# Kernel optimization log

Hardware: AMD Instinct MI355X
Metric: run time of the kernel (lower is better)

The kernel has to match this reference:

```python
import jax, jax.numpy as jnp
import numpy as np

H = 8  # num_heads
EPS = 1e-5


def layer_norm(x, g, b):
    mu = jnp.mean(x, axis=-1, keepdims=True)
    var = jnp.mean((x - mu) ** 2, axis=-1, keepdims=True)
    return (x - mu) * jax.lax.rsqrt(var + EPS) * g + b


def setup_inputs() -> dict:
    key = jax.random.key(0)
    ks = jax.random.split(key, 8)
    B, N, C = 2, 2048, 512
    Dff = 2048
    s = 0.02
    x = jax.random.normal(ks[0], (B, N, C), dtype=jnp.float32)
    mask = (jax.random.uniform(ks[1], (N, N)) > 0.5).astype(jnp.float32)
    return {
        "x": x,
        "mask": mask,
        "w_qkv": jax.random.normal(ks[2], (3 * C, C), dtype=jnp.float32) * s,
        "w_proj": jax.random.normal(ks[3], (C, C), dtype=jnp.float32) * s,
        "b_proj": jnp.zeros((C,), jnp.float32),
        "g1": jnp.ones((C,), jnp.float32),
        "beta1": jnp.zeros((C,), jnp.float32),
        "g2": jnp.ones((C,), jnp.float32),
        "beta2": jnp.zeros((C,), jnp.float32),
        "w1": jax.random.normal(ks[4], (Dff, C), dtype=jnp.float32) * s,
        "bm1": jnp.zeros((Dff,), jnp.float32),
        "w2": jax.random.normal(ks[5], (C, Dff), dtype=jnp.float32) * s,
        "bm2": jnp.zeros((C,), jnp.float32),
    }


def attn_block(h, mask, w_qkv, w_proj, b_proj):
    B, N, C = h.shape
    hd = C // H
    scale = hd ** -0.5
    qkv = (h @ w_qkv.T).reshape(B, N, 3, H, hd)
    q, k, v = jnp.moveaxis(qkv, 2, 0)          # each [B, N, H, hd]
    q = q.transpose(0, 2, 1, 3)                 # [B, H, N, hd]
    k = k.transpose(0, 2, 1, 3)
    v = v.transpose(0, 2, 1, 3)
    attn = jnp.einsum("bhnd,bhmd->bhnm", q, k) * scale
    attn = attn * mask                          # multiplicative sparse mask
    attn = jax.nn.softmax(attn, axis=-1)
    o = jnp.einsum("bhnm,bhmd->bhnd", attn, v)
    o = o.transpose(0, 2, 1, 3).reshape(B, N, C)
    return o @ w_proj.T + b_proj


def reference(x, mask, w_qkv, w_proj, b_proj, g1, beta1, g2, beta2, w1, bm1, w2, bm2):
    # pre-norm transformer block, dropout/drop_path disabled (eval)
    y = x + attn_block(layer_norm(x, g1, beta1), mask, w_qkv, w_proj, b_proj)
    h = layer_norm(y, g2, beta2)
    h = jax.nn.gelu(h @ w1.T + bm1, approximate=False)  # torch F.gelu default (erf)
    z = y + (h @ w2.T + bm2)
    return z
```

## Files before the change

kernel.cpp:

```cpp
#include <hip/hip_runtime.h>
#include <cmath>
#include <stdint.h>

#define N_SEQ 2048
#define C_DIM 512
#define BATCH 2
#define NHEAD 8
#define DFF   2048
#define M_ROWS (BATCH * N_SEQ)

typedef unsigned short ushort_t;
typedef unsigned long long u64;
typedef __bf16 bf16x8 __attribute__((ext_vector_type(8)));
typedef float  f32x4  __attribute__((ext_vector_type(4)));
typedef float  f32x16 __attribute__((ext_vector_type(16)));

__device__ __forceinline__ float bf2f(ushort_t u) {
    union { unsigned int i; float f; } v; v.i = ((unsigned int)u) << 16; return v.f;
}
__device__ __forceinline__ ushort_t f2bf_(float f) {
    union { float f; unsigned int i; } v; v.f = f;
    unsigned int r = v.i + 0x7fffu + ((v.i >> 16) & 1u);
    return (ushort_t)(r >> 16);
}
__device__ __forceinline__ unsigned short bfbits(float f) {
    return __builtin_bit_cast(unsigned short, (__bf16)f);
}
__device__ __forceinline__ int get_is32(const unsigned int* g1w) {
    return g1w[0] == 0x3F800000u;
}

__device__ __forceinline__ void load_lds16(const ushort_t* g, ushort_t* lds_wave_base) {
    __builtin_amdgcn_global_load_lds(
        (const __attribute__((address_space(1))) void*)g,
        (__attribute__((address_space(3))) void*)lds_wave_base, 16, 0, 0);
}

__device__ __forceinline__ float gelu_f(float u) {
    float c = u + 0.044715f * u * u * u;
    float E = exp2f(-2.302068545f * c);
    return u / (1.0f + E);
}

template <typename TX, typename TG>
__device__ __forceinline__ void ln_row(int row, int lane, const TX* __restrict__ x,
                                       const TG* __restrict__ g, const TG* __restrict__ b,
                                       ushort_t* __restrict__ out) {
    const TX* xr = x + (size_t)row * C_DIM + lane * 8;
    float v[8];
    if (sizeof(TX) == 2) {
        bf16x8 t = *(const bf16x8*)xr;
        #pragma unroll
        for (int j = 0; j < 8; ++j) v[j] = (float)t[j];
    } else {
        const float4* q = (const float4*)xr;
        float4 a = q[0], c = q[1];
        v[0]=a.x; v[1]=a.y; v[2]=a.z; v[3]=a.w; v[4]=c.x; v[5]=c.y; v[6]=c.z; v[7]=c.w;
    }
    float s = 0.f, sq = 0.f;
    #pragma unroll
    for (int j = 0; j < 8; ++j) { s += v[j]; sq += v[j] * v[j]; }
    #pragma unroll
    for (int m = 1; m < 64; m <<= 1) { s += __shfl_xor(s, m, 64); sq += __shfl_xor(sq, m, 64); }
    float mean = s * (1.0f / C_DIM);
    float var  = fmaxf(sq * (1.0f / C_DIM) - mean * mean, 0.0f);
    float rs = rsqrtf(var + 1e-5f);
    float gv[8], bv[8];
    const TG* gp = g + lane * 8; const TG* bp = b + lane * 8;
    if (sizeof(TG) == 2) {
        bf16x8 tg = *(const bf16x8*)gp, tb = *(const bf16x8*)bp;
        #pragma unroll
        for (int j = 0; j < 8; ++j) { gv[j] = (float)tg[j]; bv[j] = (float)tb[j]; }
    } else {
        const float4* qg = (const float4*)gp; const float4* qb = (const float4*)bp;
        float4 a=qg[0], c=qg[1], d=qb[0], e=qb[1];
        gv[0]=a.x;gv[1]=a.y;gv[2]=a.z;gv[3]=a.w;gv[4]=c.x;gv[5]=c.y;gv[6]=c.z;gv[7]=c.w;
        bv[0]=d.x;bv[1]=d.y;bv[2]=d.z;bv[3]=d.w;bv[4]=e.x;bv[5]=e.y;bv[6]=e.z;bv[7]=e.w;
    }
    bf16x8 o;
    #pragma unroll
    for (int j = 0; j < 8; ++j) o[j] = (__bf16)((v[j] - mean) * rs * gv[j] + bv[j]);
    *(bf16x8*)(out + (size_t)row * C_DIM + lane * 8) = o;
}

__global__ __launch_bounds__(256) void prep_kernel(const unsigned int* __restrict__ g1w,
        const void* w_qkv, const void* w_proj, const void* w1, const void* w2,
        const void* mask, const void* x, const void* g1, const void* b1,
        ushort_t* wq_bf, ushort_t* wp_bf, ushort_t* w1_bf, ushort_t* w2_bf,
        u64* __restrict__ maskM, ushort_t* __restrict__ hout) {
    int is32 = get_is32(g1w);
    int bid = blockIdx.x;
    int wave = threadIdx.x >> 6, lane = threadIdx.x & 63;
    if (bid < 1536) {
        long e = ((long)bid * 256 + threadIdx.x) * 8;
        const void* src; ushort_t* dst; long off;
        if      (e < 786432)  { src = w_qkv; dst = wq_bf;  off = e; }
        else if (e < 1048576) { src = w_proj; dst = wp_bf; off = e - 786432; }
        else if (e < 2097152) { src = w1;    dst = w1_bf;  off = e - 1048576; }
        else                  { src = w2;    dst = w2_bf;  off = e - 2097152; }
        bf16x8 r;
        if (is32) {
            const float4* q = (const float4*)((const float*)src + off);
            float4 a = q[0], b = q[1];
            r[0]=(__bf16)a.x; r[1]=(__bf16)a.y; r[2]=(__bf16)a.z; r[3]=(__bf16)a.w;
            r[4]=(__bf16)b.x; r[5]=(__bf16)b.y; r[6]=(__bf16)b.z; r[7]=(__bf16)b.w;
        } else {
            r = *(const bf16x8*)((const ushort_t*)src + off);
        }
        *(bf16x8*)(dst + off) = r;
    } else if (bid < 2560) {
        int pb = bid - 1536;
        #pragma unroll
        for (int it = 0; it < 16; ++it) {
            int p = pb * 64 + wave * 16 + it;
            int q = p >> 5, kb = p & 31;
            size_t idx = (size_t)q * N_SEQ + kb * 64 + lane;
            bool m = is32 ? (((const float*)mask)[idx] != 0.0f)
                          : ((((const ushort_t*)mask)[idx] & 0x7fffu) != 0);
            u64 bits = __ballot(m);
            if (lane == 0) maskM[(size_t)q * 32 + kb] = bits;
        }
    } else {
        int row = (bid - 2560) * 4 + wave;
        if (is32) ln_row<float, float>(row, lane, (const float*)x, (const float*)g1, (const float*)b1, hout);
        else      ln_row<ushort_t, ushort_t>(row, lane, (const ushort_t*)x, (const ushort_t*)g1, (const ushort_t*)b1, hout);
    }
}

__global__ __launch_bounds__(256) void ln2_kernel(const unsigned int* __restrict__ g1w,
        const ushort_t* __restrict__ y, const void* g, const void* b, ushort_t* out) {
    int row = blockIdx.x * 4 + (threadIdx.x >> 6), lane = threadIdx.x & 63;
    if (get_is32(g1w)) ln_row<ushort_t, float>(row, lane, y, (const float*)g, (const float*)b, out);
    else               ln_row<ushort_t, ushort_t>(row, lane, y, (const ushort_t*)g, (const ushort_t*)b, out);
}

template <int K, int KSPLIT, int BN, bool HAS_BIAS, int ACT, int OUT_MODE>
__global__ __launch_bounds__(256) void gemm_big(const unsigned int* __restrict__ g1w,
        const ushort_t* __restrict__ A, const ushort_t* __restrict__ W,
        const void* __restrict__ bias, void* __restrict__ Cout, int Nout) {
    constexpr int MT = (BN == 128) ? 4 : 2;
    constexpr int KL = K / KSPLIT;
    __shared__ __align__(16) ushort_t As[2][128][32];
    __shared__ __align__(16) ushort_t Bs[2][BN][32];
    int t = threadIdx.x;
    int wave = t >> 6, lane = t & 63, quad = lane >> 4, l16 = lane & 15;
    int wave_m = (BN == 128) ? (wave >> 1) : wave;
    int wave_n = (BN == 128) ? (wave & 1) : 0;
    int row0 = blockIdx.y * 128, col0 = blockIdx.x * BN;
    int kz = (KSPLIT > 1) ? blockIdx.z : 0;
    int kbase = kz * KL;

    f32x4 acc[MT][4] = {};
    int arow = t >> 2, kofs = (t & 3) * 8;

    {
        int kk = kbase + kofs;
        load_lds16(A + (size_t)(row0 + arow) * K + kk,      &As[0][0][0] + wave * 512);
        load_lds16(A + (size_t)(row0 + 64 + arow) * K + kk, &As[0][64][0] + wave * 512);
        load_lds16(W + (size_t)(col0 + arow) * K + kk,      &Bs[0][0][0] + wave * 512);
        if (BN == 128)
            load_lds16(W + (size_t)(col0 + 64 + arow) * K + kk, &Bs[0][64][0] + wave * 512);
    }
    for (int k0 = 0; k0 < KL; k0 += 32) {
        int cur = (k0 >> 5) & 1;
        __syncthreads();
        if (k0 + 32 < KL) {
            int kk = kbase + k0 + 32 + kofs;
            load_lds16(A + (size_t)(row0 + arow) * K + kk,      &As[cur ^ 1][0][0] + wave * 512);
            load_lds16(A + (size_t)(row0 + 64 + arow) * K + kk, &As[cur ^ 1][64][0] + wave * 512);
            load_lds16(W + (size_t)(col0 + arow) * K + kk,      &Bs[cur ^ 1][0][0] + wave * 512);
            if (BN == 128)
                load_lds16(W + (size_t)(col0 + 64 + arow) * K + kk, &Bs[cur ^ 1][64][0] + wave * 512);
        }
        bf16x8 af[MT], bfr[4];
        #pragma unroll
        for (int i = 0; i < MT; ++i)
            af[i] = *(const bf16x8*)&As[cur][wave_m * (MT * 16) + i * 16 + l16][quad * 8];
        #pragma unroll
        for (int j = 0; j < 4; ++j)
            bfr[j] = *(const bf16x8*)&Bs[cur][wave_n * 64 + j * 16 + l16][quad * 8];
        #pragma unroll
        for (int i = 0; i < MT; ++i)
            #pragma unroll
            for (int j = 0; j < 4; ++j)
                acc[i][j] = __builtin_amdgcn_mfma_f32_16x16x32_bf16(af[i], bfr[j], acc[i][j], 0, 0, 0);
    }

    int is32 = get_is32(g1w);
    size_t zofs = (OUT_MODE == 3) ? (size_t)kz * M_ROWS * Nout : 0;
    #pragma unroll
    for (int j = 0; j < 4; ++j) {
        int col = col0 + wave_n * 64 + j * 16 + l16;
        float bv = 0.0f;
        if (HAS_BIAS) bv = is32 ? ((const float*)bias)[col] : bf2f(((const ushort_t*)bias)[col]);
        #pragma unroll
        for (int i = 0; i < MT; ++i) {
            #pragma unroll
            for (int r = 0; r < 4; ++r) {
                int row = row0 + wave_m * (MT * 16) + i * 16 + quad * 4 + r;
                float v = acc[i][j][r] + bv;
                if (ACT == 2) v = gelu_f(v);
                size_t idx = (size_t)row * Nout + col;
                ((ushort_t*)Cout)[zofs + idx] = f2bf_(v);
            }
        }
    }
}

__global__ __launch_bounds__(256) void gemm_proj(const unsigned int* __restrict__ g1w,
        const ushort_t* __restrict__ A, const ushort_t* __restrict__ W,
        const void* __restrict__ bias, const void* __restrict__ res,
        ushort_t* __restrict__ Cout) {
    __shared__ __align__(16) ushort_t As[2][64][32];
    __shared__ __align__(16) ushort_t Bs[2][64][32];
    int t = threadIdx.x;
    int wave = t >> 6, lane = t & 63, quad = lane >> 4, l16 = lane & 15;
    int row0 = blockIdx.y * 64, col0 = blockIdx.x * 64;
    f32x4 acc[4] = {};
    int arow = t >> 2, kofs = (t & 3) * 8;

    load_lds16(A + (size_t)(row0 + arow) * 512 + kofs, &As[0][0][0] + wave * 512);
    load_lds16(W + (size_t)(col0 + arow) * 512 + kofs, &Bs[0][0][0] + wave * 512);
    for (int k0 = 0; k0 < 512; k0 += 32) {
        int cur = (k0 >> 5) & 1;
        __syncthreads();
        if (k0 + 32 < 512) {
            load_lds16(A + (size_t)(row0 + arow) * 512 + k0 + 32 + kofs, &As[cur ^ 1][0][0] + wave * 512);
            load_lds16(W + (size_t)(col0 + arow) * 512 + k0 + 32 + kofs, &Bs[cur ^ 1][0][0] + wave * 512);
        }
        bf16x8 af = *(const bf16x8*)&As[cur][wave * 16 + l16][quad * 8];
        #pragma unroll
        for (int j = 0; j < 4; ++j) {
            bf16x8 bfr = *(const bf16x8*)&Bs[cur][j * 16 + l16][quad * 8];
            acc[j] = __builtin_amdgcn_mfma_f32_16x16x32_bf16(af, bfr, acc[j], 0, 0, 0);
        }
    }
    int is32 = get_is32(g1w);
    #pragma unroll
    for (int j = 0; j < 4; ++j) {
        int col = col0 + j * 16 + l16;
        float bv = is32 ? ((const float*)bias)[col] : bf2f(((const ushort_t*)bias)[col]);
        #pragma unroll
        for (int r = 0; r < 4; ++r) {
            int row = row0 + wave * 16 + quad * 4 + r;
            size_t idx = (size_t)row * C_DIM + col;
            float v = acc[j][r] + bv;
            v += is32 ? ((const float*)res)[idx] : bf2f(((const ushort_t*)res)[idx]);
            Cout[idx] = f2bf_(v);
        }
    }
}

__global__ __launch_bounds__(256) void attn_kernel(
        const ushort_t* __restrict__ qkv, const u64* __restrict__ maskM,
        ushort_t* __restrict__ o0, ushort_t* __restrict__ o1,
        ushort_t* __restrict__ o2, ushort_t* __restrict__ o3,
        float* __restrict__ Lpart) {
    __shared__ __align__(16) ushort_t Ks[2][64][68];
    __shared__ __align__(16) ushort_t VTs[2][64][68];
    int t = threadIdx.x;
    int wave = t >> 6, lane = t & 63, l32 = lane & 31, H = lane >> 5;
    int qtile = blockIdx.x, bh = blockIdx.y, sp = blockIdx.z;
    int b = bh >> 3, h = bh & 7;
    int q = qtile * 128 + wave * 32 + l32;

    const ushort_t* base = qkv + (size_t)b * N_SEQ * 1536;
    const ushort_t* qp = base + h * 64;
    const ushort_t* kp = base + 512 + h * 64;
    const ushort_t* vp = base + 1024 + h * 64;

    const float qs = 0.125f * 1.44269504088896f;
    bf16x8 bQ[4];
    #pragma unroll
    for (int c = 0; c < 4; ++c) {
        bf16x8 raw = *(const bf16x8*)(qp + (size_t)q * 1536 + c * 16 + H * 8);
        #pragma unroll
        for (int j = 0; j < 8; ++j) bQ[c][j] = (__bf16)((float)raw[j] * qs);
    }

    int k_r = t >> 3, k_ch = (t & 7) * 8;
    int v_kp = (t & 31) * 2, v_db = (t >> 5) * 8;
    const int n_base = sp * 512;

    bf16x8 kreg[2], vreg[2];
    #pragma unroll
    for (int s = 0; s < 2; ++s)
        kreg[s] = *(const bf16x8*)(kp + (size_t)(n_base + s * 32 + k_r) * 1536 + k_ch);
    #pragma unroll
    for (int u = 0; u < 2; ++u)
        vreg[u] = *(const bf16x8*)(vp + (size_t)(n_base + v_kp + u) * 1536 + v_db);
    #pragma unroll
    for (int s = 0; s < 2; ++s)
        *(bf16x8*)&Ks[0][s * 32 + k_r][k_ch] = kreg[s];
    #pragma unroll
    for (int j = 0; j < 8; ++j) {
        unsigned int pair = (unsigned int)__builtin_bit_cast(unsigned short, vreg[0][j])
                          | ((unsigned int)__builtin_bit_cast(unsigned short, vreg[1][j]) << 16);
        *(unsigned int*)&VTs[0][v_db + j][v_kp] = pair;
    }
    u64 mw = maskM[(size_t)q * 32 + (n_base >> 6)];

    f32x16 o_acc[2] = {};
    float lsum = 0.0f;

    for (int i = 0; i < 8; ++i) {
        int n0 = n_base + i * 64;
        int cur = i & 1;
        __syncthreads();
        if (i < 7) {
            int n1 = n0 + 64;
            #pragma unroll
            for (int s = 0; s < 2; ++s)
                kreg[s] = *(const bf16x8*)(kp + (size_t)(n1 + s * 32 + k_r) * 1536 + k_ch);
            #pragma unroll
            for (int u = 0; u < 2; ++u)
                vreg[u] = *(const bf16x8*)(vp + (size_t)(n1 + v_kp + u) * 1536 + v_db);
        }
        f32x16 s_acc[2] = {};
        #pragma unroll
        for (int kt = 0; kt < 2; ++kt)
            #pragma unroll
            for (int c = 0; c < 4; ++c) {
                bf16x8 aK = *(const bf16x8*)&Ks[cur][kt * 32 + l32][c * 16 + H * 8];
                s_acc[kt] = __builtin_amdgcn_mfma_f32_32x32x16_bf16(aK, bQ[c], s_acc[kt], 0, 0, 0);
            }
        unsigned int P2[2][8];
        #pragma unroll
        for (int kt = 0; kt < 2; ++kt) {
            float p[16];
            #pragma unroll
            for (int r = 0; r < 16; ++r) {
                int keyloc = kt * 32 + (r & 3) + 8 * (r >> 2) + 4 * H;
                float e = exp2f(s_acc[kt][r]);
                p[r] = ((mw >> keyloc) & 1) ? e : 1.0f;
                lsum += p[r];
            }
            #pragma unroll
            for (int pr = 0; pr < 8; ++pr)
                P2[kt][pr] = (unsigned int)bfbits(p[2 * pr])
                           | ((unsigned int)bfbits(p[2 * pr + 1]) << 16);
        }
        if (i < 7) mw = maskM[(size_t)q * 32 + ((n0 + 64) >> 6)];
        unsigned int rv[2][4];
        #pragma unroll
        for (int kt = 0; kt < 2; ++kt)
            #pragma unroll
            for (int u = 0; u < 4; ++u) {
                int idx = (u & 1) + (u >> 1) * 4;
                unsigned int send = H ? P2[kt][idx] : P2[kt][idx + 2];
                rv[kt][u] = (unsigned int)__shfl_xor((int)send, 32, 64);
            }
        #pragma unroll
        for (int kc = 0; kc < 4; ++kc) {
            const int kt = kc >> 1, klo = kc & 1;
            union { unsigned int w[4]; bf16x8 v; } bP;
            #pragma unroll
            for (int w = 0; w < 4; ++w) {
                unsigned int own = H ? P2[kt][(w & 1) + 4 * klo + 2] : P2[kt][(w & 1) + 4 * klo];
                unsigned int oth = rv[kt][(w & 1) + 2 * klo];
                bP.w[w] = ((w >> 1) == H) ? own : oth;
            }
            #pragma unroll
            for (int dt = 0; dt < 2; ++dt) {
                bf16x8 aV = *(const bf16x8*)&VTs[cur][dt * 32 + l32][kc * 16 + H * 8];
                o_acc[dt] = __builtin_amdgcn_mfma_f32_32x32x16_bf16(aV, bP.v, o_acc[dt], 0, 0, 0);
            }
        }
        if (i < 7) {
            #pragma unroll
            for (int s = 0; s < 2; ++s)
                *(bf16x8*)&Ks[cur ^ 1][s * 32 + k_r][k_ch] = kreg[s];
            #pragma unroll
            for (int j = 0; j < 8; ++j) {
                unsigned int pair = (unsigned int)__builtin_bit_cast(unsigned short, vreg[0][j])
                                  | ((unsigned int)__builtin_bit_cast(unsigned short, vreg[1][j]) << 16);
                *(unsigned int*)&VTs[cur ^ 1][v_db + j][v_kp] = pair;
            }
        }
    }
    lsum += __shfl_xor(lsum, 32, 64);
    ushort_t* osel = (sp == 0) ? o0 : (sp == 1) ? o1 : (sp == 2) ? o2 : o3;
    ushort_t* op = osel + (size_t)bh * N_SEQ * 64;
    #pragma unroll
    for (int dt = 0; dt < 2; ++dt)
        #pragma unroll
        for (int r4 = 0; r4 < 4; ++r4) {
            int d = dt * 32 + 8 * r4 + 4 * H;
            ushort4 val;
            val.x = f2bf_(o_acc[dt][r4 * 4 + 0]);
            val.y = f2bf_(o_acc[dt][r4 * 4 + 1]);
            val.z = f2bf_(o_acc[dt][r4 * 4 + 2]);
            val.w = f2bf_(o_acc[dt][r4 * 4 + 3]);
            *(ushort4*)&op[(size_t)q * 64 + d] = val;
        }
    if (H == 0)
        Lpart[((size_t)sp * 16 + bh) * N_SEQ + q] = lsum;
}

__global__ __launch_bounds__(256) void combine_kernel(
        const ushort_t* __restrict__ o0, const ushort_t* __restrict__ o1,
        const ushort_t* __restrict__ o2, const ushort_t* __restrict__ o3,
        const float* __restrict__ Lpart, ushort_t* __restrict__ attno) {
    int gid = blockIdx.x * 256 + threadIdx.x;
    int rowg = gid >> 4;
    int dq = (gid & 15) * 4;
    int bh = rowg >> 11, qq = rowg & 2047, b = bh >> 3, h = bh & 7;
    const ushort_t* ops[4] = { o0, o1, o2, o3 };
    float acc[4] = {};
    float l = 0.0f;
    #pragma unroll
    for (int sp = 0; sp < 4; ++sp) {
        ushort4 o = *(const ushort4*)&ops[sp][(size_t)rowg * 64 + dq];
        acc[0] += bf2f(o.x); acc[1] += bf2f(o.y); acc[2] += bf2f(o.z); acc[3] += bf2f(o.w);
        l += Lpart[(size_t)sp * 16 * N_SEQ + rowg];
    }
    float inv = 1.0f / l;
    ushort4 res;
    res.x = f2bf_(acc[0] * inv); res.y = f2bf_(acc[1] * inv);
    res.z = f2bf_(acc[2] * inv); res.w = f2bf_(acc[3] * inv);
    *(ushort4*)&attno[((size_t)b * N_SEQ + qq) * C_DIM + h * 64 + dq] = res;
}

__global__ __launch_bounds__(256) void combine2_kernel(const unsigned int* __restrict__ g1w,
        const ushort_t* __restrict__ P, const ushort_t* __restrict__ y,
        const void* __restrict__ bm2, void* __restrict__ out) {
    int gid = blockIdx.x * 256 + threadIdx.x;
    size_t idx4 = (size_t)gid * 4;
    int col = (int)(idx4 & 511);
    int is32 = get_is32(g1w);
    ushort4 p0 = *(const ushort4*)&P[idx4];
    ushort4 p1 = *(const ushort4*)&P[(size_t)M_ROWS * C_DIM + idx4];
    ushort4 yv = *(const ushort4*)&y[idx4];
    float o[4];
    o[0] = bf2f(p0.x) + bf2f(p1.x) + bf2f(yv.x);
    o[1] = bf2f(p0.y) + bf2f(p1.y) + bf2f(yv.y);
    o[2] = bf2f(p0.z) + bf2f(p1.z) + bf2f(yv.z);
    o[3] = bf2f(p0.w) + bf2f(p1.w) + bf2f(yv.w);
    #pragma unroll
    for (int j = 0; j < 4; ++j)
        o[j] += is32 ? ((const float*)bm2)[col + j] : bf2f(((const ushort_t*)bm2)[col + j]);
    if (is32) {
        float4 r; r.x = o[0]; r.y = o[1]; r.z = o[2]; r.w = o[3];
        *(float4*)((float*)out + idx4) = r;
    } else {
        ushort4 r;
        r.x = f2bf_(o[0]); r.y = f2bf_(o[1]); r.z = f2bf_(o[2]); r.w = f2bf_(o[3]);
        *(ushort4*)((ushort_t*)out + idx4) = r;
    }
}

extern "C" void kernel_launch(void* const* d_in, const int* in_sizes, int n_in,
                              void* d_out, int out_size, void* d_ws, size_t ws_size,
                              hipStream_t stream) {
    char* ws = (char*)d_ws;
    const size_t KB = 1024;
    const unsigned int* g1w = (const unsigned int*)d_in[5];
    ushort_t* wq_bf = (ushort_t*)(ws);
    ushort_t* wp_bf = (ushort_t*)(ws + 1536 * KB);
    ushort_t* w1_bf = (ushort_t*)(ws + 2048 * KB);
    ushort_t* w2_bf = (ushort_t*)(ws + 4096 * KB);
    u64*      maskM = (u64*)     (ws + 6144 * KB);
    ushort_t* h     = (ushort_t*)(ws + 6656 * KB);
    ushort_t* attno = (ushort_t*)(ws + 10752 * KB);
    ushort_t* y     = (ushort_t*)(ws + 14848 * KB);
    ushort_t* qkv   = (ushort_t*)(ws + 18944 * KB);
    ushort_t* Op2   = (ushort_t*)(ws + 31232 * KB);
    ushort_t* Op3   = (ushort_t*)(ws + 35328 * KB);
    float*    Lpart = (float*)   (ws + 43520 * KB);
    ushort_t* Op0   = h;
    ushort_t* Op1   = y;
    ushort_t* gmid  = (ushort_t*)(ws + 18944 * KB);
    ushort_t* P     = (ushort_t*)(ws + 35328 * KB);

    prep_kernel<<<3584, 256, 0, stream>>>(g1w, d_in[2], d_in[3], d_in[9], d_in[11],
                                          d_in[1], d_in[0], d_in[5], d_in[6],
                                          wq_bf, wp_bf, w1_bf, w2_bf, maskM, h);
    gemm_big<512, 1, 128, false, 0, 0><<<dim3(1536 / 128, M_ROWS / 128), 256, 0, stream>>>(
        g1w, h, wq_bf, nullptr, qkv, 1536);
    attn_kernel<<<dim3(N_SEQ / 128, BATCH * NHEAD, 4), 256, 0, stream>>>(
        qkv, maskM, Op0, Op1, Op2, Op3, Lpart);
    combine_kernel<<<2048, 256, 0, stream>>>(Op0, Op1, Op2, Op3, Lpart, attno);
    gemm_proj<<<dim3(C_DIM / 64, M_ROWS / 64), 256, 0, stream>>>(
        g1w, attno, wp_bf, d_in[4], d_in[0], y);
    ln2_kernel<<<M_ROWS / 4, 256, 0, stream>>>(g1w, y, d_in[7], d_in[8], h);
    gemm_big<512, 1, 128, true, 2, 0><<<dim3(DFF / 128, M_ROWS / 128), 256, 0, stream>>>(
        g1w, h, w1_bf, d_in[10], gmid, DFF);
    gemm_big<2048, 2, 64, false, 0, 3><<<dim3(C_DIM / 64, M_ROWS / 128, 2), 256, 0, stream>>>(
        g1w, gmid, w2_bf, nullptr, P, C_DIM);
    combine2_kernel<<<2048, 256, 0, stream>>>(g1w, P, y, d_in[12], d_out);
}
```

Before: 256.4 us.

## Fuse attention split-combine into proj GEMM and split-K reduction into MLP2 GEMM

Removes the separate combine kernel by having the output projection GEMM load the four split-attention partial outputs, sum them and normalize by the summed Lpart while staging A into LDS. Replaces the split-K W2 GEMM plus combine2 kernel with a 512-thread block whose two K-halves reduce through shared memory, then add residual and bias in the epilogue. Also narrows the QKV GEMM tile to BN=64, giving it more blocks. These changes cut launches and intermediate global round-trips, at the cost of extra global loads (four partials) in the proj GEMM A path and fewer blocks for MLP2.

```diff
diff --git a/kernel.cpp b/kernel.cpp
--- a/kernel.cpp
+++ b/kernel.cpp
@@ -134,12 +134,11 @@
     else               ln_row<ushort_t, ushort_t>(row, lane, y, (const ushort_t*)g, (const ushort_t*)b, out);
 }
 
-template <int K, int KSPLIT, int BN, bool HAS_BIAS, int ACT, int OUT_MODE>
+template <int K, int BN, bool HAS_BIAS, int ACT>
 __global__ __launch_bounds__(256) void gemm_big(const unsigned int* __restrict__ g1w,
         const ushort_t* __restrict__ A, const ushort_t* __restrict__ W,
         const void* __restrict__ bias, void* __restrict__ Cout, int Nout) {
     constexpr int MT = (BN == 128) ? 4 : 2;
-    constexpr int KL = K / KSPLIT;
     __shared__ __align__(16) ushort_t As[2][128][32];
     __shared__ __align__(16) ushort_t Bs[2][BN][32];
     int t = threadIdx.x;
@@ -147,25 +146,22 @@
     int wave_m = (BN == 128) ? (wave >> 1) : wave;
     int wave_n = (BN == 128) ? (wave & 1) : 0;
     int row0 = blockIdx.y * 128, col0 = blockIdx.x * BN;
-    int kz = (KSPLIT > 1) ? blockIdx.z : 0;
-    int kbase = kz * KL;
 
     f32x4 acc[MT][4] = {};
     int arow = t >> 2, kofs = (t & 3) * 8;
 
     {
-        int kk = kbase + kofs;
-        load_lds16(A + (size_t)(row0 + arow) * K + kk,      &As[0][0][0] + wave * 512);
-        load_lds16(A + (size_t)(row0 + 64 + arow) * K + kk, &As[0][64][0] + wave * 512);
-        load_lds16(W + (size_t)(col0 + arow) * K + kk,      &Bs[0][0][0] + wave * 512);
+        load_lds16(A + (size_t)(row0 + arow) * K + kofs,      &As[0][0][0] + wave * 512);
+        load_lds16(A + (size_t)(row0 + 64 + arow) * K + kofs, &As[0][64][0] + wave * 512);
+        load_lds16(W + (size_t)(col0 + arow) * K + kofs,      &Bs[0][0][0] + wave * 512);
         if (BN == 128)
-            load_lds16(W + (size_t)(col0 + 64 + arow) * K + kk, &Bs[0][64][0] + wave * 512);
-    }
-    for (int k0 = 0; k0 < KL; k0 += 32) {
+            load_lds16(W + (size_t)(col0 + 64 + arow) * K + kofs, &Bs[0][64][0] + wave * 512);
+    }
+    for (int k0 = 0; k0 < K; k0 += 32) {
         int cur = (k0 >> 5) & 1;
         __syncthreads();
-        if (k0 + 32 < KL) {
-            int kk = kbase + k0 + 32 + kofs;
+        if (k0 + 32 < K) {
+            int kk = k0 + 32 + kofs;
             load_lds16(A + (size_t)(row0 + arow) * K + kk,      &As[cur ^ 1][0][0] + wave * 512);
             load_lds16(A + (size_t)(row0 + 64 + arow) * K + kk, &As[cur ^ 1][64][0] + wave * 512);
             load_lds16(W + (size_t)(col0 + arow) * K + kk,      &Bs[cur ^ 1][0][0] + wave * 512);
@@ -187,7 +183,6 @@
     }
 
     int is32 = get_is32(g1w);
-    size_t zofs = (OUT_MODE == 3) ? (size_t)kz * M_ROWS * Nout : 0;
     #pragma unroll
     for (int j = 0; j < 4; ++j) {
         int col = col0 + wave_n * 64 + j * 16 + l16;
@@ -200,33 +195,66 @@
                 int row = row0 + wave_m * (MT * 16) + i * 16 + quad * 4 + r;
                 float v = acc[i][j][r] + bv;
                 if (ACT == 2) v = gelu_f(v);
-                size_t idx = (size_t)row * Nout + col;
-                ((ushort_t*)Cout)[zofs + idx] = f2bf_(v);
+                ((ushort_t*)Cout)[(size_t)row * Nout + col] = f2bf_(v);
             }
         }
     }
 }
 
 __global__ __launch_bounds__(256) void gemm_proj(const unsigned int* __restrict__ g1w,
-        const ushort_t* __restrict__ A, const ushort_t* __restrict__ W,
-        const void* __restrict__ bias, const void* __restrict__ res,
-        ushort_t* __restrict__ Cout) {
+        const ushort_t* __restrict__ o0, const ushort_t* __restrict__ o1,
+        const ushort_t* __restrict__ o2, const ushort_t* __restrict__ o3,
+        const float* __restrict__ Lpart,
+        const ushort_t* __restrict__ W, const void* __restrict__ bias,
+        const void* __restrict__ res, ushort_t* __restrict__ Cout) {
     __shared__ __align__(16) ushort_t As[2][64][32];
     __shared__ __align__(16) ushort_t Bs[2][64][32];
+    __shared__ float invL[8][64];
     int t = threadIdx.x;
     int wave = t >> 6, lane = t & 63, quad = lane >> 4, l16 = lane & 15;
     int row0 = blockIdx.y * 64, col0 = blockIdx.x * 64;
+    int arow = t >> 2, kofs = (t & 3) * 8;
+    int row_t = row0 + arow, b_ = row_t >> 11, q_ = row_t & 2047;
+
+    #pragma unroll
+    for (int e = t; e < 512; e += 256) {
+        int hh = e >> 6, ql = e & 63;
+        int row = row0 + ql;
+        size_t rg = (size_t)(((row >> 11) * 8 + hh)) * 2048 + (row & 2047);
+        float l = Lpart[rg] + Lpart[32768 + rg] + Lpart[65536 + rg] + Lpart[98304 + rg];
+        invL[hh][ql] = 1.0f / l;
+    }
+
+    auto loadA = [&](int k0, bf16x8* a) {
+        int hh = k0 >> 6;
+        int d = (k0 & 63) + kofs;
+        size_t rg = ((size_t)(b_ * 8 + hh) * 2048 + q_) * 64 + d;
+        a[0] = *(const bf16x8*)(o0 + rg);
+        a[1] = *(const bf16x8*)(o1 + rg);
+        a[2] = *(const bf16x8*)(o2 + rg);
+        a[3] = *(const bf16x8*)(o3 + rg);
+    };
+    auto writeA = [&](int k0, int buf, bf16x8* a) {
+        float inv = invL[k0 >> 6][arow];
+        bf16x8 av;
+        #pragma unroll
+        for (int j = 0; j < 8; ++j)
+            av[j] = (__bf16)(((float)a[0][j] + (float)a[1][j] + (float)a[2][j] + (float)a[3][j]) * inv);
+        *(bf16x8*)&As[buf][arow][kofs] = av;
+    };
+
     f32x4 acc[4] = {};
-    int arow = t >> 2, kofs = (t & 3) * 8;
-
-    load_lds16(A + (size_t)(row0 + arow) * 512 + kofs, &As[0][0][0] + wave * 512);
+    bf16x8 areg[4];
     load_lds16(W + (size_t)(col0 + arow) * 512 + kofs, &Bs[0][0][0] + wave * 512);
+    loadA(0, areg);
+    __syncthreads();
+    writeA(0, 0, areg);
     for (int k0 = 0; k0 < 512; k0 += 32) {
         int cur = (k0 >> 5) & 1;
         __syncthreads();
         if (k0 + 32 < 512) {
-            load_lds16(A + (size_t)(row0 + arow) * 512 + k0 + 32 + kofs, &As[cur ^ 1][0][0] + wave * 512);
             load_lds16(W + (size_t)(col0 + arow) * 512 + k0 + 32 + kofs, &Bs[cur ^ 1][0][0] + wave * 512);
+            loadA(k0 + 32, areg);
         }
         bf16x8 af = *(const bf16x8*)&As[cur][wave * 16 + l16][quad * 8];
         #pragma unroll
@@ -234,6 +262,8 @@
             bf16x8 bfr = *(const bf16x8*)&Bs[cur][j * 16 + l16][quad * 8];
             acc[j] = __builtin_amdgcn_mfma_f32_16x16x32_bf16(af, bfr, acc[j], 0, 0, 0);
         }
+        if (k0 + 32 < 512)
+            writeA(k0 + 32, cur ^ 1, areg);
     }
     int is32 = get_is32(g1w);
     #pragma unroll
@@ -247,6 +277,87 @@
             float v = acc[j][r] + bv;
             v += is32 ? ((const float*)res)[idx] : bf2f(((const ushort_t*)res)[idx]);
             Cout[idx] = f2bf_(v);
+        }
+    }
+}
+
+__global__ __launch_bounds__(512) void gemm_mlp2(const unsigned int* __restrict__ g1w,
+        const ushort_t* __restrict__ A, const ushort_t* __restrict__ W,
+        const ushort_t* __restrict__ y, const void* __restrict__ bm2,
+        void* __restrict__ out) {
+    __shared__ __align__(16) char smem[49152];
+    int t = threadIdx.x;
+    int kg = t >> 8, tl = t & 255;
+    int wave = tl >> 6, lane = t & 63, quad = lane >> 4, l16 = lane & 15;
+    int row0 = blockIdx.y * 128, col0 = blockIdx.x * 64;
+    int kbase = kg * 1024;
+    int arow = tl >> 2, kofs = (tl & 3) * 8;
+
+    f32x4 acc[2][4] = {};
+    {
+        int kk = kbase + kofs;
+        ushort_t* As0 = (ushort_t*)(smem + ((size_t)kg * 2 + 0) * 8192);
+        ushort_t* Bs0 = (ushort_t*)(smem + 32768 + ((size_t)kg * 2 + 0) * 4096);
+        load_lds16(A + (size_t)(row0 + arow) * DFF + kk,      As0 + wave * 512);
+        load_lds16(A + (size_t)(row0 + 64 + arow) * DFF + kk, As0 + 2048 + wave * 512);
+        load_lds16(W + (size_t)(col0 + arow) * DFF + kk,      Bs0 + wave * 512);
+    }
+    for (int k0 = 0; k0 < 1024; k0 += 32) {
+        int cur = (k0 >> 5) & 1;
+        __syncthreads();
+        if (k0 + 32 < 1024) {
+            int kk = kbase + k0 + 32 + kofs;
+            ushort_t* Asn = (ushort_t*)(smem + ((size_t)kg * 2 + (cur ^ 1)) * 8192);
+            ushort_t* Bsn = (ushort_t*)(smem + 32768 + ((size_t)kg * 2 + (cur ^ 1)) * 4096);
+            load_lds16(A + (size_t)(row0 + arow) * DFF + kk,      Asn + wave * 512);
+            load_lds16(A + (size_t)(row0 + 64 + arow) * DFF + kk, Asn + 2048 + wave * 512);
+            load_lds16(W + (size_t)(col0 + arow) * DFF + kk,      Bsn + wave * 512);
+        }
+        const ushort_t* Asc = (const ushort_t*)(smem + ((size_t)kg * 2 + cur) * 8192);
+        const ushort_t* Bsc = (const ushort_t*)(smem + 32768 + ((size_t)kg * 2 + cur) * 4096);
+        bf16x8 af[2], bfr[4];
+        #pragma unroll
+        for (int i = 0; i < 2; ++i)
+            af[i] = *(const bf16x8*)&Asc[(wave * 32 + i * 16 + l16) * 32 + quad * 8];
+        #pragma unroll
+        for (int j = 0; j < 4; ++j)
+            bfr[j] = *(const bf16x8*)&Bsc[(j * 16 + l16) * 32 + quad * 8];
+        #pragma unroll
+        for (int i = 0; i < 2; ++i)
+            #pragma unroll
+            for (int j = 0; j < 4; ++j)
+                acc[i][j] = __builtin_amdgcn_mfma_f32_16x16x32_bf16(af[i], bfr[j], acc[i][j], 0, 0, 0);
+    }
+    __syncthreads();
+    float* scr = (float*)smem;
+    if (kg == 1) {
+        #pragma unroll
+        for (int i = 0; i < 2; ++i)
+            #pragma unroll
+            for (int j = 0; j < 4; ++j)
+                #pragma unroll
+                for (int r = 0; r < 4; ++r)
+                    scr[(wave * 32 + i * 16 + quad * 4 + r) * 64 + j * 16 + l16] = acc[i][j][r];
+    }
+    __syncthreads();
+    if (kg == 0) {
+        int is32 = get_is32(g1w);
+        #pragma unroll
+        for (int j = 0; j < 4; ++j) {
+            int col = col0 + j * 16 + l16;
+            float bm = is32 ? ((const float*)bm2)[col] : bf2f(((const ushort_t*)bm2)[col]);
+            #pragma unroll
+            for (int i = 0; i < 2; ++i) {
+                #pragma unroll
+                for (int r = 0; r < 4; ++r) {
+                    int rl = wave * 32 + i * 16 + quad * 4 + r;
+                    int row = row0 + rl;
+                    size_t idx = (size_t)row * C_DIM + col;
+                    float v = acc[i][j][r] + scr[rl * 64 + j * 16 + l16] + bf2f(y[idx]) + bm;
+                    if (is32) ((float*)out)[idx] = v;
+                    else      ((ushort_t*)out)[idx] = f2bf_(v);
+                }
+            }
         }
     }
 }
@@ -397,58 +508,6 @@
         Lpart[((size_t)sp * 16 + bh) * N_SEQ + q] = lsum;
 }
 
-__global__ __launch_bounds__(256) void combine_kernel(
-        const ushort_t* __restrict__ o0, const ushort_t* __restrict__ o1,
-        const ushort_t* __restrict__ o2, const ushort_t* __restrict__ o3,
-        const float* __restrict__ Lpart, ushort_t* __restrict__ attno) {
-    int gid = blockIdx.x * 256 + threadIdx.x;
-    int rowg = gid >> 4;
-    int dq = (gid & 15) * 4;
-    int bh = rowg >> 11, qq = rowg & 2047, b = bh >> 3, h = bh & 7;
-    const ushort_t* ops[4] = { o0, o1, o2, o3 };
-    float acc[4] = {};
-    float l = 0.0f;
-    #pragma unroll
-    for (int sp = 0; sp < 4; ++sp) {
-        ushort4 o = *(const ushort4*)&ops[sp][(size_t)rowg * 64 + dq];
-        acc[0] += bf2f(o.x); acc[1] += bf2f(o.y); acc[2] += bf2f(o.z); acc[3] += bf2f(o.w);
-        l += Lpart[(size_t)sp * 16 * N_SEQ + rowg];
-    }
-    float inv = 1.0f / l;
-    ushort4 res;
-    res.x = f2bf_(acc[0] * inv); res.y = f2bf_(acc[1] * inv);
-    res.z = f2bf_(acc[2] * inv); res.w = f2bf_(acc[3] * inv);
-    *(ushort4*)&attno[((size_t)b * N_SEQ + qq) * C_DIM + h * 64 + dq] = res;
-}
-
-__global__ __launch_bounds__(256) void combine2_kernel(const unsigned int* __restrict__ g1w,
-        const ushort_t* __restrict__ P, const ushort_t* __restrict__ y,
-        const void* __restrict__ bm2, void* __restrict__ out) {
-    int gid = blockIdx.x * 256 + threadIdx.x;
-    size_t idx4 = (size_t)gid * 4;
-    int col = (int)(idx4 & 511);
-    int is32 = get_is32(g1w);
-    ushort4 p0 = *(const ushort4*)&P[idx4];
-    ushort4 p1 = *(const ushort4*)&P[(size_t)M_ROWS * C_DIM + idx4];
-    ushort4 yv = *(const ushort4*)&y[idx4];
-    float o[4];
-    o[0] = bf2f(p0.x) + bf2f(p1.x) + bf2f(yv.x);
-    o[1] = bf2f(p0.y) + bf2f(p1.y) + bf2f(yv.y);
-    o[2] = bf2f(p0.z) + bf2f(p1.z) + bf2f(yv.z);
-    o[3] = bf2f(p0.w) + bf2f(p1.w) + bf2f(yv.w);
-    #pragma unroll
-    for (int j = 0; j < 4; ++j)
-        o[j] += is32 ? ((const float*)bm2)[col + j] : bf2f(((const ushort_t*)bm2)[col + j]);
-    if (is32) {
-        float4 r; r.x = o[0]; r.y = o[1]; r.z = o[2]; r.w = o[3];
-        *(float4*)((float*)out + idx4) = r;
-    } else {
-        ushort4 r;
-        r.x = f2bf_(o[0]); r.y = f2bf_(o[1]); r.z = f2bf_(o[2]); r.w = f2bf_(o[3]);
-        *(ushort4*)((ushort_t*)out + idx4) = r;
-    }
-}
-
 extern "C" void kernel_launch(void* const* d_in, const int* in_sizes, int n_in,
                               void* d_out, int out_size, void* d_ws, size_t ws_size,
                               hipStream_t stream) {
@@ -461,31 +520,27 @@
     ushort_t* w2_bf = (ushort_t*)(ws + 4096 * KB);
     u64*      maskM = (u64*)     (ws + 6144 * KB);
     ushort_t* h     = (ushort_t*)(ws + 6656 * KB);
-    ushort_t* attno = (ushort_t*)(ws + 10752 * KB);
+    ushort_t* Op1   = (ushort_t*)(ws + 10752 * KB);
     ushort_t* y     = (ushort_t*)(ws + 14848 * KB);
     ushort_t* qkv   = (ushort_t*)(ws + 18944 * KB);
     ushort_t* Op2   = (ushort_t*)(ws + 31232 * KB);
     ushort_t* Op3   = (ushort_t*)(ws + 35328 * KB);
     float*    Lpart = (float*)   (ws + 43520 * KB);
     ushort_t* Op0   = h;
-    ushort_t* Op1   = y;
     ushort_t* gmid  = (ushort_t*)(ws + 18944 * KB);
-    ushort_t* P     = (ushort_t*)(ws + 35328 * KB);
 
     prep_kernel<<<3584, 256, 0, stream>>>(g1w, d_in[2], d_in[3], d_in[9], d_in[11],
                                           d_in[1], d_in[0], d_in[5], d_in[6],
                                           wq_bf, wp_bf, w1_bf, w2_bf, maskM, h);
-    gemm_big<512, 1, 128, false, 0, 0><<<dim3(1536 / 128, M_ROWS / 128), 256, 0, stream>>>(
+    gemm_big<512, 64, false, 0><<<dim3(1536 / 64, M_ROWS / 128), 256, 0, stream>>>(
         g1w, h, wq_bf, nullptr, qkv, 1536);
     attn_kernel<<<dim3(N_SEQ / 128, BATCH * NHEAD, 4), 256, 0, stream>>>(
         qkv, maskM, Op0, Op1, Op2, Op3, Lpart);
-    combine_kernel<<<2048, 256, 0, stream>>>(Op0, Op1, Op2, Op3, Lpart, attno);
     gemm_proj<<<dim3(C_DIM / 64, M_ROWS / 64), 256, 0, stream>>>(
-        g1w, attno, wp_bf, d_in[4], d_in[0], y);
+        g1w, Op0, Op1, Op2, Op3, Lpart, wp_bf, d_in[4], d_in[0], y);
     ln2_kernel<<<M_ROWS / 4, 256, 0, stream>>>(g1w, y, d_in[7], d_in[8], h);
-    gemm_big<512, 1, 128, true, 2, 0><<<dim3(DFF / 128, M_ROWS / 128), 256, 0, stream>>>(
+    gemm_big<512, 128, true, 2><<<dim3(DFF / 128, M_ROWS / 128), 256, 0, stream>>>(
         g1w, h, w1_bf, d_in[10], gmid, DFF);
-    gemm_big<2048, 2, 64, false, 0, 3><<<dim3(C_DIM / 64, M_ROWS / 128, 2), 256, 0, stream>>>(
-        g1w, gmid, w2_bf, nullptr, P, C_DIM);
-    combine2_kernel<<<2048, 256, 0, stream>>>(g1w, P, y, d_in[12], d_out);
-}
+    gemm_mlp2<<<dim3(C_DIM / 64, M_ROWS / 128), 512, 0, stream>>>(
+        g1w, gmid, w2_bf, y, d_in[12], d_out);
+}
```

New measurement: 265.3 us. +3.4%, slower.
